# Optimization experiments

Measured on AMD Instinct MI355X. Metric: run time of the kernel, lower is better.

The kernel has to match this reference:

```python
import jax, jax.numpy as jnp
import numpy as np

N_SPACE = 197  # spatial tokens (ViT-B/16: 196 patches + CLS)
T = 8          # frames, fixed by space_time_pos shape (197*8, dim)
H = 12         # heads


def setup_inputs() -> dict:
    key = jax.random.key(0)
    ks = jax.random.split(key, 8)
    dim = 768
    B = 8
    Nq = 1576
    scale = dim ** -0.5
    return {
        "s_x": jax.random.normal(ks[0], (N_SPACE, B * T, dim), jnp.float32),
        "t_x": jax.random.normal(ks[1], (B, Nq, dim), jnp.float32),
        "space_time_pos": scale * jax.random.normal(ks[2], (N_SPACE * T, dim), jnp.float32),
        "q_w": jax.random.normal(ks[3], (dim, dim), jnp.float32) * 0.02,
        "q_b": jnp.zeros((dim,), jnp.float32),
        "kv_w": jax.random.normal(ks[4], (2 * dim, dim), jnp.float32) * 0.02,
        "kv_b": jnp.zeros((2 * dim,), jnp.float32),
        "proj_w": jax.random.normal(ks[5], (dim, dim), jnp.float32) * 0.02,
        "proj_b": jnp.zeros((dim,), jnp.float32),
    }


def reference(s_x, t_x, space_time_pos, q_w, q_b, kv_w, kv_b, proj_w, proj_b):
    n, BT, dim = s_x.shape
    B, Nq, _ = t_x.shape
    t = BT // B
    head_dim = dim // H
    scale = head_dim ** -0.5

    # rearrange 'n (b t) d -> b (t n) d'
    s = s_x.reshape(n, B, t, dim).transpose(1, 2, 0, 3).reshape(B, t * n, dim)
    s = s + space_time_pos  # (B, t*n, dim)

    # Q from t_x, K/V from s
    q = t_x @ q_w.T + q_b                      # (B, Nq, dim)
    kv = s @ kv_w.T + kv_b                     # (B, t*n, 2*dim)
    Nk = t * n
    # 'b n (e h d) -> e b h n d'
    kv = kv.reshape(B, Nk, 2, H, head_dim).transpose(2, 0, 3, 1, 4)
    k, v = kv[0], kv[1]                        # (B, H, Nk, hd)
    q = q.reshape(B, Nq, H, head_dim).transpose(0, 2, 1, 3) * scale  # (B, H, Nq, hd)

    attn = jnp.einsum('bhqd,bhkd->bhqk', q, k)
    attn = jax.nn.softmax(attn, axis=-1)
    out = jnp.einsum('bhqk,bhkd->bhqd', attn, v)   # (B, H, Nq, hd)
    out = out.transpose(0, 2, 1, 3).reshape(B, Nq, dim)
    return out @ proj_w.T + proj_b
```

## Files before the change

### kernel.cpp

```cpp
#include <hip/hip_runtime.h>
#include <stdint.h>

#define NSPACE 197
#define TFRAMES 8
#define NH 12
#define DIM 768
#define HD 64
#define BATCH 8
#define NQ 1576
#define NK 1576
#define M_REAL 12608
#define M_PAD 12672
#define VT_LD 1600

typedef __attribute__((ext_vector_type(8))) short s16x8;
typedef __attribute__((ext_vector_type(4))) short s16x4;
typedef __attribute__((ext_vector_type(4))) float f32x4;

__device__ inline uint16_t f2bf(float f) {
    union { float f; uint32_t i; } c; c.f = f;
    uint32_t r = c.i + 0x7FFF + ((c.i >> 16) & 1);
    return (uint16_t)(r >> 16);
}

__device__ inline uint32_t cvtpk_bf16(float lo, float hi) {
    uint32_t r;
    asm("v_cvt_pk_bf16_f32 %0, %1, %2" : "=v"(r) : "v"(lo), "v"(hi));
    return r;
}

__device__ inline float exp2_raw(float x) { return __builtin_amdgcn_exp2f(x); }

__device__ inline void gld_lds16(const uint16_t* g, uint16_t* l) {
    __builtin_amdgcn_global_load_lds(
        (const __attribute__((address_space(1))) void*)g,
        (__attribute__((address_space(3))) void*)l,
        16, 0, 0);
}


__global__ void conv_f2b(const float* __restrict__ src, uint16_t* __restrict__ dst, int n8) {
    int chunk = blockIdx.x * 256 + threadIdx.x;
    if (chunk >= n8) return;
    size_t off = (size_t)chunk * 8;
    float4 a = *(const float4*)(src + off);
    float4 b = *(const float4*)(src + off + 4);
    union { s16x8 v; uint32_t u[4]; } o;
    o.u[0] = cvtpk_bf16(a.x, a.y);
    o.u[1] = cvtpk_bf16(a.z, a.w);
    o.u[2] = cvtpk_bf16(b.x, b.y);
    o.u[3] = cvtpk_bf16(b.z, b.w);
    *(s16x8*)(dst + off) = o.v;
}

__global__ void fill_x(const float* __restrict__ t_x, uint16_t* __restrict__ x_pad) {
    int chunk = blockIdx.x * 256 + threadIdx.x;
    const int total = M_PAD * (DIM / 8);
    if (chunk >= total) return;
    size_t off = (size_t)chunk * 8;
    s16x8 o;
    if (off < (size_t)M_REAL * DIM) {
        float4 a = *(const float4*)(t_x + off);
        float4 b = *(const float4*)(t_x + off + 4);
        union { s16x8 v; uint32_t u[4]; } p;
        p.u[0] = cvtpk_bf16(a.x, a.y);
        p.u[1] = cvtpk_bf16(a.z, a.w);
        p.u[2] = cvtpk_bf16(b.x, b.y);
        p.u[3] = cvtpk_bf16(b.z, b.w);
        o = p.v;
    } else {
        for (int j = 0; j < 8; j++) o[j] = 0;
    }
    *(s16x8*)(x_pad + off) = o;
}

__global__ void fill_s(const float* __restrict__ s_x, const float* __restrict__ pos,
                       uint16_t* __restrict__ s_pad) {
    int chunk = blockIdx.x * 256 + threadIdx.x;
    const int total = M_PAD * (DIM / 8);
    if (chunk >= total) return;
    int i = chunk / (DIM / 8);
    int cc = chunk - i * (DIM / 8);
    int d0 = cc * 8;
    uint16_t* dst = s_pad + (size_t)i * DIM + d0;
    if (i >= M_REAL) {
        s16x8 z; for (int j = 0; j < 8; j++) z[j] = 0;
        *(s16x8*)dst = z;
        return;
    }
    int b = i / NK, rr = i - b * NK;
    int t_i = rr / NSPACE, n_i = rr - t_i * NSPACE;
    const float* src = s_x + ((size_t)(n_i * (BATCH * TFRAMES) + b * TFRAMES + t_i)) * DIM + d0;
    const float* ps = pos + (size_t)rr * DIM + d0;
    float4 a0 = *(const float4*)src;
    float4 a1 = *(const float4*)(src + 4);
    float4 p0 = *(const float4*)ps;
    float4 p1 = *(const float4*)(ps + 4);
    union { s16x8 v; uint32_t u[4]; } o;
    o.u[0] = cvtpk_bf16(a0.x + p0.x, a0.y + p0.y);
    o.u[1] = cvtpk_bf16(a0.z + p0.z, a0.w + p0.w);
    o.u[2] = cvtpk_bf16(a1.x + p1.x, a1.y + p1.y);
    o.u[3] = cvtpk_bf16(a1.z + p1.z, a1.w + p1.w);
    *(s16x8*)dst = o.v;
}

template <int MODE>
__global__ __launch_bounds__(256)
void gemm_bt(const uint16_t* __restrict__ A, const uint16_t* __restrict__ W,
             const float* __restrict__ bias,
             uint16_t* __restrict__ out0, uint16_t* __restrict__ out1,
             float* __restrict__ outf) {
    __shared__ uint16_t As[128 * 32];
    __shared__ uint16_t Bs[128 * 32];
    const int t = threadIdx.x;
    const int lane = t & 63, w = t >> 6;
    const int r16 = lane & 15, quad = lane >> 4;
    const int wm = w >> 1, wn = w & 1;
    const int m0 = blockIdx.y * 128;
    const int n0 = blockIdx.x * 128;

    const int srow = w * 32 + (lane >> 2);
    const int scol = (lane & 3) * 8;
    const uint16_t* Ag = A + (size_t)(m0 + srow) * DIM + scol;
    const uint16_t* Wg = W + (size_t)(n0 + srow) * DIM + scol;
    uint16_t* Asw = &As[w * 32 * 32];
    uint16_t* Bsw = &Bs[w * 32 * 32];

    f32x4 acc[4][4];
    for (int a = 0; a < 4; a++)
        for (int bb = 0; bb < 4; bb++)
            for (int r = 0; r < 4; r++) acc[a][bb][r] = 0.f;

    for (int kk = 0; kk < DIM; kk += 32) {
        gld_lds16(Ag + kk, Asw);
        gld_lds16(Ag + kk + (size_t)16 * DIM, Asw + 16 * 32);
        gld_lds16(Wg + kk, Bsw);
        gld_lds16(Wg + kk + (size_t)16 * DIM, Bsw + 16 * 32);
        __syncthreads();
        s16x8 af[4], bfr[4];
        for (int mt = 0; mt < 4; mt++)
            af[mt] = *(const s16x8*)&As[(wm * 64 + mt * 16 + r16) * 32 + quad * 8];
        for (int nt = 0; nt < 4; nt++)
            bfr[nt] = *(const s16x8*)&Bs[(wn * 64 + nt * 16 + r16) * 32 + quad * 8];
        for (int mt = 0; mt < 4; mt++)
            for (int nt = 0; nt < 4; nt++)
                acc[mt][nt] = __builtin_amdgcn_mfma_f32_16x16x32_bf16(af[mt], bfr[nt], acc[mt][nt], 0, 0, 0);
        __syncthreads();
    }

    for (int mt = 0; mt < 4; mt++)
        for (int nt = 0; nt < 4; nt++) {
            int col = n0 + wn * 64 + nt * 16 + r16;
            float bz = bias[col];
            int rowb = m0 + wm * 64 + mt * 16 + quad * 4;
            for (int r = 0; r < 4; r++) {
                int i = rowb + r;
                if (i >= M_REAL) continue;
                float v = acc[mt][nt][r] + bz;
                if (MODE == 0) {
                    int b = i / NQ, nq = i - b * NQ;
                    int h = col >> 6, d = col & 63;
                    out0[(size_t)(((b * NH + h) * NQ) + nq) * HD + d] = f2bf(v * 0.18033688011112042f);
                } else if (MODE == 1) {
                    int b = i / NK, nk = i - b * NK;
                    if (col < DIM) {
                        int h = col >> 6, d = col & 63;
                        out0[(size_t)(((b * NH + h) * NK) + nk) * HD + d] = f2bf(v);
                    } else {
                        int c2 = col - DIM;
                        int h = c2 >> 6, d = c2 & 63;
                        out1[(size_t)(((b * NH + h) * NK) + nk) * HD + d] = f2bf(v);
                    }
                } else {
                    outf[(size_t)i * DIM + col] = v;
                }
            }
        }
}

__global__ __launch_bounds__(256)
void transpose_v(const uint16_t* __restrict__ v, uint16_t* __restrict__ vt) {
    __shared__ uint16_t T[64 * 72];
    int tile = blockIdx.x, bh = blockIdx.y;
    int nk0 = tile * 64;
    const uint16_t* V = v + (size_t)bh * NK * HD;
    uint16_t* VT = vt + (size_t)bh * HD * VT_LD;
    int tid = threadIdx.x;
    int rr = tid >> 3;
    int c8 = (tid & 7) * 8;
    for (int p = 0; p < 2; p++) {
        int lr = p * 32 + rr;
        int nk = nk0 + lr;
        s16x8 val;
        if (nk < NK) val = *(const s16x8*)(V + (size_t)nk * HD + c8);
        else for (int j = 0; j < 8; j++) val[j] = 0;
        for (int j = 0; j < 8; j++)
            T[(c8 + j) * 72 + lr] = (uint16_t)val[j];
    }
    __syncthreads();
    for (int p = 0; p < 2; p++) {
        int d = p * 32 + rr;
        s16x8 o = *(const s16x8*)&T[d * 72 + c8];
        *(s16x8*)(VT + (size_t)d * VT_LD + nk0 + c8) = o;
    }
}

#define NITER 50
__global__ __launch_bounds__(256)
void flash_attn(const uint16_t* __restrict__ q_buf, const uint16_t* __restrict__ k_buf,
                const uint16_t* __restrict__ vt_buf, uint16_t* __restrict__ ao) {
    __shared__ uint16_t Kb[2][32 * 72];
    __shared__ uint16_t Vb[2][64 * 40];
    int h = blockIdx.y, b = blockIdx.z;
    int tid = threadIdx.x;
    int lane = tid & 63, w = tid >> 6;
    int r16 = lane & 15, quad = lane >> 4;
    size_t bh = (size_t)(b * NH + h);
    const uint16_t* Q = q_buf + bh * NQ * HD;
    const uint16_t* K = k_buf + bh * NK * HD;
    const uint16_t* VT = vt_buf + bh * HD * VT_LD;
    int q0 = blockIdx.x * 128 + w * 32;

    const int kg = tid >> 3;
    const int kc = (tid & 7) * 8;
    const int kslot = ((kg >> 3) << 2) + (kg & 3) + ((kg & 4) ? 16 : 0);
    const int vd = tid >> 2;
    const int vc = (tid & 3) * 8;
    const uint16_t* Kg = K + (size_t)kg * HD + kc;
    const uint16_t* Vg = VT + (size_t)vd * VT_LD + vc;
    uint16_t* Kw = &Kb[0][kslot * 72 + kc];
    uint16_t* Vw = &Vb[0][vd * 40 + vc];
    const int KBSZ = 32 * 72, VBSZ = 64 * 40;

    s16x8 qf[2][2];
    for (int m = 0; m < 2; m++) {
        int qrow = q0 + m * 16 + r16;
        if (qrow < NQ) {
            qf[m][0] = *(const s16x8*)(Q + (size_t)qrow * HD + quad * 8);
            qf[m][1] = *(const s16x8*)(Q + (size_t)qrow * HD + 32 + quad * 8);
        } else {
            for (int j = 0; j < 8; j++) { qf[m][0][j] = 0; qf[m][1][j] = 0; }
        }
    }

    f32x4 z4;
    for (int r = 0; r < 4; r++) z4[r] = 0.f;

    f32x4 oT[2][4];
    f32x4 lsum4[2];
    for (int m = 0; m < 2; m++) {
        for (int dt = 0; dt < 4; dt++)
            for (int r = 0; r < 4; r++) oT[m][dt][r] = 0.f;
        for (int r = 0; r < 4; r++) lsum4[m][r] = 0.f;
    }

    {
        s16x8 kv = *(const s16x8*)Kg;
        s16x8 vv = *(const s16x8*)Vg;
        *(s16x8*)Kw = kv;
        *(s16x8*)Vw = vv;
    }
    __syncthreads();

    for (int it = 0; it < NITER - 1; it++) {
        int kb = it * 32;
        int cur = it & 1, nxt = cur ^ 1;
        s16x8 knv = *(const s16x8*)(Kg + (size_t)(kb + 32) * HD);
        s16x8 vnv = *(const s16x8*)(Vg + kb + 32);

        const uint16_t* Kc = &Kb[cur][0];
        const uint16_t* Vc = &Vb[cur][0];
        s16x8 kfA0 = *(const s16x8*)(Kc + r16 * 72 + quad * 8);
        s16x8 kfA1 = *(const s16x8*)(Kc + r16 * 72 + 32 + quad * 8);
        s16x8 kfB0 = *(const s16x8*)(Kc + (16 + r16) * 72 + quad * 8);
        s16x8 kfB1 = *(const s16x8*)(Kc + (16 + r16) * 72 + 32 + quad * 8);

        s16x8 pf[2];
        #pragma unroll
        for (int m = 0; m < 2; m++) {
            f32x4 sA = __builtin_amdgcn_mfma_f32_16x16x32_bf16(kfA0, qf[m][0], z4, 0, 0, 0);
            sA = __builtin_amdgcn_mfma_f32_16x16x32_bf16(kfA1, qf[m][1], sA, 0, 0, 0);
            f32x4 sB = __builtin_amdgcn_mfma_f32_16x16x32_bf16(kfB0, qf[m][0], z4, 0, 0, 0);
            sB = __builtin_amdgcn_mfma_f32_16x16x32_bf16(kfB1, qf[m][1], sB, 0, 0, 0);
            f32x4 pA, pB;
            #pragma unroll
            for (int r = 0; r < 4; r++) { pA[r] = exp2_raw(sA[r]); pB[r] = exp2_raw(sB[r]); }
            lsum4[m] += pA;
            lsum4[m] += pB;
            union { s16x8 v; uint32_t u[4]; } pk;
            pk.u[0] = cvtpk_bf16(pA[0], pA[1]);
            pk.u[1] = cvtpk_bf16(pA[2], pA[3]);
            pk.u[2] = cvtpk_bf16(pB[0], pB[1]);
            pk.u[3] = cvtpk_bf16(pB[2], pB[3]);
            pf[m] = pk.v;
        }
        #pragma unroll
        for (int dt = 0; dt < 4; dt++) {
            s16x8 vf = *(const s16x8*)(Vc + (dt * 16 + r16) * 40 + quad * 8);
            oT[0][dt] = __builtin_amdgcn_mfma_f32_16x16x32_bf16(vf, pf[0], oT[0][dt], 0, 0, 0);
            oT[1][dt] = __builtin_amdgcn_mfma_f32_16x16x32_bf16(vf, pf[1], oT[1][dt], 0, 0, 0);
        }
        *(s16x8*)(Kw + nxt * KBSZ) = knv;
        *(s16x8*)(Vw + nxt * VBSZ) = vnv;
        __syncthreads();
    }

    {
        const int it = NITER - 1;
        const int kb = it * 32;
        const int cur = it & 1;
        const uint16_t* Kc = &Kb[cur][0];
        const uint16_t* Vc = &Vb[cur][0];
        s16x8 kfA0 = *(const s16x8*)(Kc + r16 * 72 + quad * 8);
        s16x8 kfA1 = *(const s16x8*)(Kc + r16 * 72 + 32 + quad * 8);
        s16x8 kfB0 = *(const s16x8*)(Kc + (16 + r16) * 72 + quad * 8);
        s16x8 kfB1 = *(const s16x8*)(Kc + (16 + r16) * 72 + 32 + quad * 8);

        s16x8 pf[2];
        #pragma unroll
        for (int m = 0; m < 2; m++) {
            f32x4 sA = __builtin_amdgcn_mfma_f32_16x16x32_bf16(kfA0, qf[m][0], z4, 0, 0, 0);
            sA = __builtin_amdgcn_mfma_f32_16x16x32_bf16(kfA1, qf[m][1], sA, 0, 0, 0);
            f32x4 sB = __builtin_amdgcn_mfma_f32_16x16x32_bf16(kfB0, qf[m][0], z4, 0, 0, 0);
            sB = __builtin_amdgcn_mfma_f32_16x16x32_bf16(kfB1, qf[m][1], sB, 0, 0, 0);
            f32x4 pA, pB;
            #pragma unroll
            for (int r = 0; r < 4; r++) {
                pA[r] = (kb + quad * 8 + r < NK)     ? exp2_raw(sA[r]) : 0.f;
                pB[r] = (kb + quad * 8 + 4 + r < NK) ? exp2_raw(sB[r]) : 0.f;
            }
            lsum4[m] += pA;
            lsum4[m] += pB;
            union { s16x8 v; uint32_t u[4]; } pk;
            pk.u[0] = cvtpk_bf16(pA[0], pA[1]);
            pk.u[1] = cvtpk_bf16(pA[2], pA[3]);
            pk.u[2] = cvtpk_bf16(pB[0], pB[1]);
            pk.u[3] = cvtpk_bf16(pB[2], pB[3]);
            pf[m] = pk.v;
        }
        #pragma unroll
        for (int dt = 0; dt < 4; dt++) {
            s16x8 vf = *(const s16x8*)(Vc + (dt * 16 + r16) * 40 + quad * 8);
            oT[0][dt] = __builtin_amdgcn_mfma_f32_16x16x32_bf16(vf, pf[0], oT[0][dt], 0, 0, 0);
            oT[1][dt] = __builtin_amdgcn_mfma_f32_16x16x32_bf16(vf, pf[1], oT[1][dt], 0, 0, 0);
        }
    }

    #pragma unroll
    for (int m = 0; m < 2; m++) {
        float rs = lsum4[m][0] + lsum4[m][1] + lsum4[m][2] + lsum4[m][3];
        rs += __shfl_xor(rs, 16);
        rs += __shfl_xor(rs, 32);
        int q = q0 + m * 16 + r16;
        if (q >= NQ) continue;
        float inv = 1.0f / rs;
        size_t rowoff = (size_t)(b * NQ + q) * DIM + h * HD;
        #pragma unroll
        for (int dt = 0; dt < 4; dt++) {
            union { s16x4 v; uint32_t u[2]; } o;
            o.u[0] = cvtpk_bf16(oT[m][dt][0] * inv, oT[m][dt][1] * inv);
            o.u[1] = cvtpk_bf16(oT[m][dt][2] * inv, oT[m][dt][3] * inv);
            *(s16x4*)(ao + rowoff + dt * 16 + quad * 4) = o.v;
        }
    }
}

extern "C" void kernel_launch(void* const* d_in, const int* in_sizes, int n_in,
                              void* d_out, int out_size, void* d_ws, size_t ws_size,
                              hipStream_t stream) {
    const float* s_x    = (const float*)d_in[0];
    const float* t_x    = (const float*)d_in[1];
    const float* pos    = (const float*)d_in[2];
    const float* q_w    = (const float*)d_in[3];
    const float* q_b    = (const float*)d_in[4];
    const float* kv_w   = (const float*)d_in[5];
    const float* kv_b   = (const float*)d_in[6];
    const float* proj_w = (const float*)d_in[7];
    const float* proj_b = (const float*)d_in[8];
    float* out = (float*)d_out;

    char* ws = (char*)d_ws;
    size_t off = 0;
    auto carve = [&](size_t bytes) {
        void* p = ws + off;
        off += (bytes + 255) & ~(size_t)255;
        return p;
    };
    uint16_t* x_pad  = (uint16_t*)carve((size_t)M_PAD * DIM * 2);
    uint16_t* s_pad  = (uint16_t*)carve((size_t)M_PAD * DIM * 2);
    uint16_t* q_buf  = (uint16_t*)carve((size_t)BATCH * NH * NQ * HD * 2);
    uint16_t* k_buf  = (uint16_t*)carve((size_t)BATCH * NH * NK * HD * 2);
    uint16_t* vt_buf = (uint16_t*)carve((size_t)BATCH * NH * HD * VT_LD * 2);
    uint16_t* wbuf   = (uint16_t*)carve((size_t)2 * DIM * DIM * 2);
    if (off > ws_size) return;
    uint16_t* v_buf = x_pad;
    uint16_t* ao    = x_pad;

    const int fill_blocks = (M_PAD * (DIM / 8) + 255) / 256;
    const int wq8 = DIM * DIM / 8, wkv8 = 2 * DIM * DIM / 8;

    fill_x<<<fill_blocks, 256, 0, stream>>>(t_x, x_pad);
    fill_s<<<fill_blocks, 256, 0, stream>>>(s_x, pos, s_pad);

    conv_f2b<<<(wq8 + 255) / 256, 256, 0, stream>>>(q_w, wbuf, wq8);
    gemm_bt<0><<<dim3(DIM / 128, M_PAD / 128), 256, 0, stream>>>(x_pad, wbuf, q_b, q_buf, nullptr, nullptr);

    conv_f2b<<<(wkv8 + 255) / 256, 256, 0, stream>>>(kv_w, wbuf, wkv8);
    gemm_bt<1><<<dim3(2 * DIM / 128, M_PAD / 128), 256, 0, stream>>>(s_pad, wbuf, kv_b, k_buf, v_buf, nullptr);
    transpose_v<<<dim3(VT_LD / 64, BATCH * NH), 256, 0, stream>>>(v_buf, vt_buf);

    flash_attn<<<dim3((NQ + 127) / 128, NH, BATCH), 256, 0, stream>>>(q_buf, k_buf, vt_buf, ao);

    conv_f2b<<<(wq8 + 255) / 256, 256, 0, stream>>>(proj_w, wbuf, wq8);
    gemm_bt<2><<<dim3(DIM / 128, M_PAD / 128), 256, 0, stream>>>(ao, wbuf, proj_b, nullptr, nullptr, out);
}
```

Baseline: 367.2 us.

## Double-buffer LDS tiles in projection GEMM to overlap loads with MFMA

Doubles the shared-memory A/B tiles in the bt GEMM and issues the global-to-LDS loads for the next K slice before computing on the current one. This hides global load latency behind MFMA work and halves the barriers per K step. LDS use per block doubles to 32KB, which may lower occupancy. Correctness depends on the async LDS loads completing before each barrier.

```diff
diff --git a/kernel.cpp b/kernel.cpp
--- a/kernel.cpp
+++ b/kernel.cpp
@@ -110,8 +110,8 @@
              const float* __restrict__ bias,
              uint16_t* __restrict__ out0, uint16_t* __restrict__ out1,
              float* __restrict__ outf) {
-    __shared__ uint16_t As[128 * 32];
-    __shared__ uint16_t Bs[128 * 32];
+    __shared__ uint16_t As[2][128 * 32];
+    __shared__ uint16_t Bs[2][128 * 32];
     const int t = threadIdx.x;
     const int lane = t & 63, w = t >> 6;
     const int r16 = lane & 15, quad = lane >> 4;
@@ -123,28 +123,43 @@
     const int scol = (lane & 3) * 8;
     const uint16_t* Ag = A + (size_t)(m0 + srow) * DIM + scol;
     const uint16_t* Wg = W + (size_t)(n0 + srow) * DIM + scol;
-    uint16_t* Asw = &As[w * 32 * 32];
-    uint16_t* Bsw = &Bs[w * 32 * 32];
+    const int lbase = w * 32 * 32;
 
     f32x4 acc[4][4];
     for (int a = 0; a < 4; a++)
         for (int bb = 0; bb < 4; bb++)
             for (int r = 0; r < 4; r++) acc[a][bb][r] = 0.f;
 
-    for (int kk = 0; kk < DIM; kk += 32) {
-        gld_lds16(Ag + kk, Asw);
-        gld_lds16(Ag + kk + (size_t)16 * DIM, Asw + 16 * 32);
-        gld_lds16(Wg + kk, Bsw);
-        gld_lds16(Wg + kk + (size_t)16 * DIM, Bsw + 16 * 32);
-        __syncthreads();
+    auto stage = [&](int kkoff, int buf) {
+        gld_lds16(Ag + kkoff, &As[buf][lbase]);
+        gld_lds16(Ag + kkoff + (size_t)16 * DIM, &As[buf][lbase + 16 * 32]);
+        gld_lds16(Wg + kkoff, &Bs[buf][lbase]);
+        gld_lds16(Wg + kkoff + (size_t)16 * DIM, &Bs[buf][lbase + 16 * 32]);
+    };
+    auto compute = [&](int buf) {
         s16x8 af[4], bfr[4];
+        #pragma unroll
         for (int mt = 0; mt < 4; mt++)
-            af[mt] = *(const s16x8*)&As[(wm * 64 + mt * 16 + r16) * 32 + quad * 8];
+            af[mt] = *(const s16x8*)&As[buf][(wm * 64 + mt * 16 + r16) * 32 + quad * 8];
+        #pragma unroll
         for (int nt = 0; nt < 4; nt++)
-            bfr[nt] = *(const s16x8*)&Bs[(wn * 64 + nt * 16 + r16) * 32 + quad * 8];
+            bfr[nt] = *(const s16x8*)&Bs[buf][(wn * 64 + nt * 16 + r16) * 32 + quad * 8];
+        #pragma unroll
         for (int mt = 0; mt < 4; mt++)
+            #pragma unroll
             for (int nt = 0; nt < 4; nt++)
                 acc[mt][nt] = __builtin_amdgcn_mfma_f32_16x16x32_bf16(af[mt], bfr[nt], acc[mt][nt], 0, 0, 0);
+    };
+
+    stage(0, 0);
+    __syncthreads();
+
+    for (int kk = 0; kk < DIM; kk += 64) {
+        stage(kk + 32, 1);
+        compute(0);
+        __syncthreads();
+        if (kk + 64 < DIM) stage(kk + 64, 0);
+        compute(1);
         __syncthreads();
     }
 
```

Result: no change. 367.9 us (+0.2%).
